# Kernel tuning notes

Hardware: AMD Instinct MI355X
Metric: run time of the kernel (lower is better)

The kernel has to match this reference:

```python
import jax, jax.numpy as jnp
import numpy as np
import math

N_NODES = 25000
N_EDGES = 400000
FEAT = 128
N_RBF = 20
CUTOFF = 5.0
EPS = 1e-15


def setup_inputs() -> dict:
    key = jax.random.key(0)
    ks = jax.random.split(key, 10)
    s_j = jax.random.normal(ks[0], (N_NODES, FEAT), dtype=jnp.float32)
    v_j = jax.random.normal(ks[1], (N_NODES, FEAT, 3), dtype=jnp.float32)
    r_ij = jax.random.normal(ks[2], (N_EDGES, 3), dtype=jnp.float32)
    nbrs = jax.random.randint(ks[3], (N_EDGES, 2), 0, N_NODES, dtype=jnp.int64)
    # InvariantDense: Linear(F,F) -> swish -> Linear(F,3F)
    sc1 = 1.0 / math.sqrt(FEAT)
    W1 = jax.random.uniform(ks[4], (FEAT, FEAT), jnp.float32, -sc1, sc1)
    b1 = jnp.zeros((FEAT,), jnp.float32)
    W2 = jax.random.uniform(ks[5], (FEAT, 3 * FEAT), jnp.float32, -sc1, sc1)
    b2 = jnp.zeros((3 * FEAT,), jnp.float32)
    # DistanceEmbed dense: Linear(n_rbf, 3F)
    scd = 1.0 / math.sqrt(N_RBF)
    Wd = jax.random.uniform(ks[6], (N_RBF, 3 * FEAT), jnp.float32, -scd, scd)
    bd = jnp.zeros((3 * FEAT,), jnp.float32)
    return {"s_j": s_j, "v_j": v_j, "r_ij": r_ij, "nbrs": nbrs,
            "W1": W1, "b1": b1, "W2": W2, "b2": b2, "Wd": Wd, "bd": bd}


def _swish(x):
    return x * jax.nn.sigmoid(x)


def reference(s_j, v_j, r_ij, nbrs, W1, b1, W2, b2, Wd, bd):
    # preprocess_r
    dist = jnp.sqrt(jnp.sum(r_ij * r_ij + EPS, axis=-1))        # [E]
    unit = r_ij / dist[:, None]                                  # [E, 3]

    src = nbrs[:, 1]
    dst = nbrs[:, 0]

    # invariant dense on gathered scalar features
    s_nb = s_j[src]                                              # [E, F]
    phi = _swish(s_nb @ W1 + b1) @ W2 + b2                       # [E, 3F]

    # radial basis: sin(n*pi*d/cutoff)/d, n = 1..n_rbf
    n = jnp.arange(1, N_RBF + 1, dtype=jnp.float32)
    rbf = jnp.sin(n * jnp.pi / CUTOFF * dist[:, None]) / dist[:, None]  # [E, n_rbf]
    w_s = rbf @ Wd + bd                                          # [E, 3F]

    inv = (phi * w_s).reshape(-1, FEAT, 3)                       # [E, F, 3]
    split0 = inv[:, :, 0:1]                                      # [E, F, 1]
    split1 = inv[:, :, 1]                                        # [E, F]
    split2 = inv[:, :, 2:3]                                      # [E, F, 1]

    delta_v_ij = split2 * unit[:, None, :] + split0 * v_j[src]   # [E, F, 3]
    delta_s_ij = split1                                          # [E, F]

    delta_s_i = jax.ops.segment_sum(delta_s_ij, dst, num_segments=s_j.shape[0])
    delta_v_i = jax.ops.segment_sum(delta_v_ij, dst, num_segments=s_j.shape[0])
    return (delta_s_i, delta_v_i)
```

## Files before the change

### kernel.cpp

```cpp
#include <hip/hip_runtime.h>

namespace {

constexpr int FEAT   = 128;
constexpr int NRBF   = 20;
constexpr int EPB    = 32;
constexpr int NNODES = 25000;
constexpr int NEDGES = 400000;
constexpr int NBLK   = NEDGES / EPB;
constexpr int NSCAN  = (NNODES + 255) / 256;
constexpr float PI_F = 3.14159265358979323846f;

using f32x4 = __attribute__((ext_vector_type(4))) float;
using s16x8 = __attribute__((ext_vector_type(8))) short;
using s16x4 = __attribute__((ext_vector_type(4))) short;

constexpr int PW1_ELEMS = 8  * 4 * 64 * 8;
constexpr int PW2_ELEMS = 24 * 4 * 64 * 8;
constexpr int PWD_ELEMS = 24 * 1 * 64 * 8;
constexpr int PW1_OFF = 0;
constexpr int PW2_OFF = PW1_ELEMS;
constexpr int PWD_OFF = PW1_ELEMS + PW2_ELEMS;
constexpr int PT_TOTAL = PW1_ELEMS + PW2_ELEMS + PWD_ELEMS;

__device__ inline unsigned short f2bf(float f) {
    unsigned u = __builtin_bit_cast(unsigned, f);
    u += 0x7fffu + ((u >> 16) & 1u);
    return (unsigned short)(u >> 16);
}
__device__ inline float bf2f(unsigned short h) {
    unsigned u = ((unsigned)h) << 16;
    return __builtin_bit_cast(float, u);
}

__global__ __launch_bounds__(256) void prep_kernel(
    const float* __restrict__ W1, const float* __restrict__ W2,
    const float* __restrict__ Wd, short* __restrict__ pw)
{
    const int idx = blockIdx.x * 256 + threadIdx.x;
    if (idx >= PT_TOTAL) return;
    float val;
    if (idx < PW2_OFF) {
        const int t = idx;
        const int r = t & 7, lane = (t >> 3) & 63, ks = (t >> 9) & 3, nt = t >> 11;
        const int k = ks*32 + (lane>>4)*8 + r, n = nt*16 + (lane & 15);
        val = W1[k*128 + n];
    } else if (idx < PWD_OFF) {
        const int t = idx - PW2_OFF;
        const int r = t & 7, lane = (t >> 3) & 63, ks = (t >> 9) & 3, nt = t >> 11;
        const int k = ks*32 + (lane>>4)*8 + r, n = nt*16 + (lane & 15);
        const int orig = 3*(n & 127) + (n >> 7);
        val = W2[k*384 + orig];
    } else {
        const int t = idx - PWD_OFF;
        const int r = t & 7, lane = (t >> 3) & 63, nt = t >> 9;
        const int k = (lane>>4)*8 + r, n = nt*16 + (lane & 15);
        const int orig = 3*(n & 127) + (n >> 7);
        val = (k < NRBF) ? Wd[k*384 + orig] : 0.f;
    }
    pw[idx] = (short)f2bf(val);
}

__global__ __launch_bounds__(256) void hist_kernel(
    const int* __restrict__ nbrs, int* __restrict__ hist)
{
    const int e = blockIdx.x * 256 + threadIdx.x;
    if (e >= NEDGES) return;
    const int2 nb = reinterpret_cast<const int2*>(nbrs)[e];
    atomicAdd(&hist[nb.x], 1);
}

__global__ __launch_bounds__(256) void scanA_kernel(
    const int* __restrict__ hist, int* __restrict__ cursor, int* __restrict__ bsum)
{
    __shared__ int sh[256];
    const int t = threadIdx.x, idx = blockIdx.x*256 + t;
    const int v = (idx < NNODES) ? hist[idx] : 0;
    sh[t] = v; __syncthreads();
    int acc = v;
    for (int off = 1; off < 256; off <<= 1) {
        const int add = (t >= off) ? sh[t-off] : 0;
        __syncthreads();
        acc += add; sh[t] = acc;
        __syncthreads();
    }
    if (idx < NNODES) cursor[idx] = acc - v;
    if (t == 255) bsum[blockIdx.x] = acc;
}

__global__ __launch_bounds__(128) void scanB_kernel(
    const int* __restrict__ bsum, int* __restrict__ boffs)
{
    __shared__ int sh[128];
    const int t = threadIdx.x;
    const int v = (t < NSCAN) ? bsum[t] : 0;
    sh[t] = v; __syncthreads();
    int acc = v;
    for (int off = 1; off < 128; off <<= 1) {
        const int add = (t >= off) ? sh[t-off] : 0;
        __syncthreads();
        acc += add; sh[t] = acc;
        __syncthreads();
    }
    if (t < NSCAN) boffs[t] = acc - v;
}

__global__ __launch_bounds__(256) void scanC_kernel(
    int* __restrict__ cursor, const int* __restrict__ boffs)
{
    const int idx = blockIdx.x*256 + threadIdx.x;
    if (idx < NNODES) cursor[idx] += boffs[blockIdx.x];
}

__global__ __launch_bounds__(256) void scatter_kernel(
    const int* __restrict__ nbrs, int* __restrict__ cursor,
    int* __restrict__ eids)
{
    const int e = blockIdx.x * 256 + threadIdx.x;
    if (e >= NEDGES) return;
    const int dst = nbrs[2*e];
    const int pos = atomicAdd(&cursor[dst], 1);
    eids[pos] = e;
}

__global__ __launch_bounds__(256) void msg_kernel(
    const float* __restrict__ s_j, const float* __restrict__ v_j,
    const float* __restrict__ r_ij, const int* __restrict__ nbrs,
    const float* __restrict__ b1, const float* __restrict__ b2,
    const float* __restrict__ bd, const short* __restrict__ pw,
    const int* __restrict__ eids,
    float* __restrict__ ds_out, float* __restrict__ dv_out)
{
    __shared__ short sTile[12288];
    __shared__ float sU[EPB][3];
    __shared__ int   sSrc[EPB], sDst[EPB];
    constexpr int OFF_A = 0, OFF_H = 4096, OFF_R = 8192;

    const int tid = threadIdx.x;
    const int w   = tid >> 6;
    const int l   = tid & 63;
    const int mr  = l & 15;
    const int g   = l >> 4;
    const int e0  = blockIdx.x * EPB;

    {
        const int ep  = tid >> 3;
        const int sub = tid & 7;
        const int eid = eids[e0 + ep];
        const int2 nb = reinterpret_cast<const int2*>(nbrs)[eid];
        const float r0 = r_ij[3*eid+0], r1 = r_ij[3*eid+1], r2 = r_ij[3*eid+2];
        const float d     = sqrtf(r0*r0 + r1*r1 + r2*r2 + 3e-15f);
        const float inv_d = 1.0f / d;
        if (sub == 0) {
            sDst[ep] = nb.x; sSrc[ep] = nb.y;
            sU[ep][0] = r0*inv_d; sU[ep][1] = r1*inv_d; sU[ep][2] = r2*inv_d;
        }
        s16x8 rv;
        #pragma unroll
        for (int kk = 0; kk < 8; ++kk) {
            const int k = sub*8 + kk;
            const float v = (k < NRBF) ? __sinf((float)(k+1)*(PI_F/5.0f)*d)*inv_d : 0.f;
            rv[kk] = (short)f2bf(v);
        }
        *reinterpret_cast<s16x8*>(&sTile[OFF_R + ep*64 + ((sub*8) ^ ((ep & 7) << 3))]) = rv;
    }

    #pragma unroll
    for (int p = 0; p < 4; ++p) {
        const int v  = tid + p*256;
        const int e  = v >> 5;
        const int c4 = (v & 31) * 4;
        const int eid = eids[e0 + e];
        const int src = nbrs[2*eid + 1];
        const float4 f = reinterpret_cast<const float4*>(s_j + (size_t)src*FEAT)[v & 31];
        s16x4 h;
        h.x = (short)f2bf(f.x); h.y = (short)f2bf(f.y);
        h.z = (short)f2bf(f.z); h.w = (short)f2bf(f.w);
        *reinterpret_cast<s16x4*>(&sTile[OFF_A + e*128 + (c4 ^ ((e & 7) << 3))]) = h;
    }
    __syncthreads();

    {
        s16x8 aS[2][4];
        #pragma unroll
        for (int mt = 0; mt < 2; ++mt) {
            const int m = mt*16 + mr;
            const int xr = (m & 7) << 3;
            #pragma unroll
            for (int ks = 0; ks < 4; ++ks)
                aS[mt][ks] = *reinterpret_cast<const s16x8*>(&sTile[OFF_A + m*128 + ((ks*32 + g*8) ^ xr)]);
        }
        const s16x8* pW1 = reinterpret_cast<const s16x8*>(pw + PW1_OFF);
        #pragma unroll
        for (int i = 0; i < 2; ++i) {
            const int nt = w*2 + i;
            const int n  = nt*16 + mr;
            const float b1n = b1[n];
            f32x4 acc[2] = {f32x4{0,0,0,0}, f32x4{0,0,0,0}};
            #pragma unroll
            for (int ks = 0; ks < 4; ++ks) {
                const s16x8 b = pW1[(nt*4 + ks)*64 + l];
                acc[0] = __builtin_amdgcn_mfma_f32_16x16x32_bf16(aS[0][ks], b, acc[0], 0, 0, 0);
                acc[1] = __builtin_amdgcn_mfma_f32_16x16x32_bf16(aS[1][ks], b, acc[1], 0, 0, 0);
            }
            #pragma unroll
            for (int mt = 0; mt < 2; ++mt)
                #pragma unroll
                for (int r = 0; r < 4; ++r) {
                    const int m = mt*16 + g*4 + r;
                    const float x = acc[mt][r] + b1n;
                    const float hsw = x / (1.0f + __expf(-x));
                    sTile[OFF_H + m*128 + (n ^ ((m & 7) << 3))] = (short)f2bf(hsw);
                }
        }
    }
    __syncthreads();

    {
        s16x8 aH[2][4], aR[2];
        #pragma unroll
        for (int mt = 0; mt < 2; ++mt) {
            const int m = mt*16 + mr;
            const int xr = (m & 7) << 3;
            #pragma unroll
            for (int ks = 0; ks < 4; ++ks)
                aH[mt][ks] = *reinterpret_cast<const s16x8*>(&sTile[OFF_H + m*128 + ((ks*32 + g*8) ^ xr)]);
            aR[mt] = *reinterpret_cast<const s16x8*>(&sTile[OFF_R + m*64 + ((g*8) ^ xr)]);
        }
        __syncthreads();

        const s16x8* pW2 = reinterpret_cast<const s16x8*>(pw + PW2_OFF);
        const s16x8* pWd = reinterpret_cast<const s16x8*>(pw + PWD_OFF);
        #pragma unroll
        for (int i = 0; i < 6; ++i) {
            const int nt = w*6 + i;
            const int n  = nt*16 + mr;
            const int c  = n >> 7;
            const int f2 = n & 127;
            const int orig = 3*f2 + c;
            const float b2n = b2[orig], bdn = bd[orig];
            f32x4 acc[2]  = {f32x4{0,0,0,0}, f32x4{0,0,0,0}};
            f32x4 accw[2] = {f32x4{0,0,0,0}, f32x4{0,0,0,0}};
            #pragma unroll
            for (int ks = 0; ks < 4; ++ks) {
                const s16x8 b = pW2[(nt*4 + ks)*64 + l];
                acc[0] = __builtin_amdgcn_mfma_f32_16x16x32_bf16(aH[0][ks], b, acc[0], 0, 0, 0);
                acc[1] = __builtin_amdgcn_mfma_f32_16x16x32_bf16(aH[1][ks], b, acc[1], 0, 0, 0);
            }
            const s16x8 bw = pWd[nt*64 + l];
            accw[0] = __builtin_amdgcn_mfma_f32_16x16x32_bf16(aR[0], bw, accw[0], 0, 0, 0);
            accw[1] = __builtin_amdgcn_mfma_f32_16x16x32_bf16(aR[1], bw, accw[1], 0, 0, 0);
            #pragma unroll
            for (int mt = 0; mt < 2; ++mt)
                #pragma unroll
                for (int r = 0; r < 4; ++r) {
                    const int m = mt*16 + g*4 + r;
                    const float inv = (acc[mt][r] + b2n) * (accw[mt][r] + bdn);
                    sTile[c*4096 + m*128 + (f2 ^ ((m & 7) << 3))] = (short)f2bf(inv);
                }
        }
    }
    __syncthreads();

    {
        const int half = tid >> 7;
        const int f    = tid & 127;
        const int eb   = half * 16;
        float accS = 0.f, a0 = 0.f, a1 = 0.f, a2 = 0.f;
        int cur = sDst[eb];
        #pragma unroll 4
        for (int e = eb; e < eb + 16; ++e) {
            const int d = sDst[e];
            if (d != cur) {
                atomicAdd(ds_out + (size_t)cur*FEAT + f, accS);
                float* dvp = dv_out + (size_t)cur*(3*FEAT) + 3*f;
                atomicAdd(dvp + 0, a0);
                atomicAdd(dvp + 1, a1);
                atomicAdd(dvp + 2, a2);
                accS = a0 = a1 = a2 = 0.f;
                cur = d;
            }
            const int fx = f ^ ((e & 7) << 3);
            const float i0 = bf2f((unsigned short)sTile[        e*128 + fx]);
            const float i1 = bf2f((unsigned short)sTile[4096 + e*128 + fx]);
            const float i2 = bf2f((unsigned short)sTile[8192 + e*128 + fx]);
            const int src = sSrc[e];
            const float* vj = v_j + (size_t)src*(3*FEAT) + 3*f;
            const float u0 = sU[e][0], u1 = sU[e][1], u2 = sU[e][2];
            accS += i1;
            a0 += i2*u0 + i0*vj[0];
            a1 += i2*u1 + i0*vj[1];
            a2 += i2*u2 + i0*vj[2];
        }
        atomicAdd(ds_out + (size_t)cur*FEAT + f, accS);
        float* dvp = dv_out + (size_t)cur*(3*FEAT) + 3*f;
        atomicAdd(dvp + 0, a0);
        atomicAdd(dvp + 1, a1);
        atomicAdd(dvp + 2, a2);
    }
}

}

extern "C" void kernel_launch(void* const* d_in, const int* in_sizes, int n_in,
                              void* d_out, int out_size, void* d_ws, size_t ws_size,
                              hipStream_t stream)
{
    const float* s_j  = (const float*)d_in[0];
    const float* v_j  = (const float*)d_in[1];
    const float* r_ij = (const float*)d_in[2];
    const int*   nbrs = (const int*)d_in[3];
    const float* W1   = (const float*)d_in[4];
    const float* b1   = (const float*)d_in[5];
    const float* W2   = (const float*)d_in[6];
    const float* b2   = (const float*)d_in[7];
    const float* Wd   = (const float*)d_in[8];
    const float* bd   = (const float*)d_in[9];

    float* ds_out = (float*)d_out;
    float* dv_out = ds_out + (size_t)NNODES * FEAT;

    char* base   = (char*)d_ws;
    short* pw    = (short*)base;
    int*  hist   = (int*)(base + 160*1024);
    int*  cursor = (int*)(base + 272*1024);
    int*  bsum   = (int*)(base + 376*1024);
    int*  boffs  = (int*)(base + 380*1024);
    int*  eids   = (int*)(base + 384*1024);

    hipMemsetAsync(d_out, 0, (size_t)out_size * sizeof(float), stream);
    hipMemsetAsync(hist, 0, NNODES * sizeof(int), stream);

    prep_kernel<<<(PT_TOTAL + 255)/256, 256, 0, stream>>>(W1, W2, Wd, pw);
    hist_kernel<<<(NEDGES + 255)/256, 256, 0, stream>>>(nbrs, hist);
    scanA_kernel<<<NSCAN, 256, 0, stream>>>(hist, cursor, bsum);
    scanB_kernel<<<1, 128, 0, stream>>>(bsum, boffs);
    scanC_kernel<<<NSCAN, 256, 0, stream>>>(cursor, boffs);
    scatter_kernel<<<(NEDGES + 255)/256, 256, 0, stream>>>(nbrs, cursor, eids);

    msg_kernel<<<NBLK, 256, 0, stream>>>(
        s_j, v_j, r_ij, nbrs, b1, b2, bd, pw, eids, ds_out, dv_out);
}
```

Baseline: 438.2 us.

## Compute phi per node instead of per edge and pre-sort edge records

```diff
diff --git a/kernel.cpp b/kernel.cpp
--- a/kernel.cpp
+++ b/kernel.cpp
@@ -8,6 +8,7 @@
 constexpr int NNODES = 25000;
 constexpr int NEDGES = 400000;
 constexpr int NBLK   = NEDGES / EPB;
+constexpr int NPBLK  = (NNODES + 31) / 32;
 constexpr int NSCAN  = (NNODES + 255) / 256;
 constexpr float PI_F = 3.14159265358979323846f;
 
@@ -61,6 +62,111 @@
     pw[idx] = (short)f2bf(val);
 }
 
+__global__ __launch_bounds__(256) void nodephi_kernel(
+    const float* __restrict__ s_j, const float* __restrict__ b1,
+    const float* __restrict__ b2, const short* __restrict__ pw,
+    unsigned short* __restrict__ phiT)
+{
+    __shared__ short sT[8192];
+    constexpr int OFF_H = 4096;
+    const int tid = threadIdx.x;
+    const int w   = tid >> 6;
+    const int l   = tid & 63;
+    const int mr  = l & 15;
+    const int g   = l >> 4;
+    const int n0  = blockIdx.x * 32;
+
+    #pragma unroll
+    for (int p = 0; p < 4; ++p) {
+        const int v  = tid + p*256;
+        const int e  = v >> 5;
+        const int c4 = (v & 31) * 4;
+        const int node = n0 + e;
+        float4 f = {0.f, 0.f, 0.f, 0.f};
+        if (node < NNODES)
+            f = reinterpret_cast<const float4*>(s_j + (size_t)node*FEAT)[v & 31];
+        s16x4 h;
+        h.x = (short)f2bf(f.x); h.y = (short)f2bf(f.y);
+        h.z = (short)f2bf(f.z); h.w = (short)f2bf(f.w);
+        *reinterpret_cast<s16x4*>(&sT[e*128 + (c4 ^ ((e & 7) << 3))]) = h;
+    }
+    __syncthreads();
+
+    {
+        s16x8 aS[2][4];
+        #pragma unroll
+        for (int mt = 0; mt < 2; ++mt) {
+            const int m = mt*16 + mr;
+            const int xr = (m & 7) << 3;
+            #pragma unroll
+            for (int ks = 0; ks < 4; ++ks)
+                aS[mt][ks] = *reinterpret_cast<const s16x8*>(&sT[m*128 + ((ks*32 + g*8) ^ xr)]);
+        }
+        const s16x8* pW1 = reinterpret_cast<const s16x8*>(pw + PW1_OFF);
+        #pragma unroll
+        for (int i = 0; i < 2; ++i) {
+            const int nt = w*2 + i;
+            const int n  = nt*16 + mr;
+            const float b1n = b1[n];
+            f32x4 acc[2] = {f32x4{0,0,0,0}, f32x4{0,0,0,0}};
+            #pragma unroll
+            for (int ks = 0; ks < 4; ++ks) {
+                const s16x8 b = pW1[(nt*4 + ks)*64 + l];
+                acc[0] = __builtin_amdgcn_mfma_f32_16x16x32_bf16(aS[0][ks], b, acc[0], 0, 0, 0);
+                acc[1] = __builtin_amdgcn_mfma_f32_16x16x32_bf16(aS[1][ks], b, acc[1], 0, 0, 0);
+            }
+            #pragma unroll
+            for (int mt = 0; mt < 2; ++mt)
+                #pragma unroll
+                for (int r = 0; r < 4; ++r) {
+                    const int m = mt*16 + g*4 + r;
+                    const float x = acc[mt][r] + b1n;
+                    const float hsw = x / (1.0f + __expf(-x));
+                    sT[OFF_H + m*128 + (n ^ ((m & 7) << 3))] = (short)f2bf(hsw);
+                }
+        }
+    }
+    __syncthreads();
+
+    {
+        s16x8 aH[2][4];
+        #pragma unroll
+        for (int mt = 0; mt < 2; ++mt) {
+            const int m = mt*16 + mr;
+            const int xr = (m & 7) << 3;
+            #pragma unroll
+            for (int ks = 0; ks < 4; ++ks)
+                aH[mt][ks] = *reinterpret_cast<const s16x8*>(&sT[OFF_H + m*128 + ((ks*32 + g*8) ^ xr)]);
+        }
+        const s16x8* pW2 = reinterpret_cast<const s16x8*>(pw + PW2_OFF);
+        #pragma unroll
+        for (int i = 0; i < 6; ++i) {
+            const int nt = w*6 + i;
+            const int n  = nt*16 + mr;
+            const int c  = n >> 7;
+            const int f2 = n & 127;
+            const float b2n = b2[3*f2 + c];
+            f32x4 acc[2] = {f32x4{0,0,0,0}, f32x4{0,0,0,0}};
+            #pragma unroll
+            for (int ks = 0; ks < 4; ++ks) {
+                const s16x8 b = pW2[(nt*4 + ks)*64 + l];
+                acc[0] = __builtin_amdgcn_mfma_f32_16x16x32_bf16(aH[0][ks], b, acc[0], 0, 0, 0);
+                acc[1] = __builtin_amdgcn_mfma_f32_16x16x32_bf16(aH[1][ks], b, acc[1], 0, 0, 0);
+            }
+            #pragma unroll
+            for (int mt = 0; mt < 2; ++mt)
+                #pragma unroll
+                for (int r = 0; r < 4; ++r) {
+                    const int m = mt*16 + g*4 + r;
+                    const int node = n0 + m;
+                    if (node < NNODES)
+                        phiT[(size_t)c*NNODES*FEAT + (size_t)node*FEAT + f2] =
+                            f2bf(acc[mt][r] + b2n);
+                }
+        }
+    }
+}
+
 __global__ __launch_bounds__(256) void hist_kernel(
     const int* __restrict__ nbrs, int* __restrict__ hist)
 {
@@ -113,28 +219,27 @@
 }
 
 __global__ __launch_bounds__(256) void scatter_kernel(
-    const int* __restrict__ nbrs, int* __restrict__ cursor,
-    int* __restrict__ eids)
+    const int* __restrict__ nbrs, const float* __restrict__ r_ij,
+    int* __restrict__ cursor, int2* __restrict__ recDS, float4* __restrict__ recR)
 {
     const int e = blockIdx.x * 256 + threadIdx.x;
     if (e >= NEDGES) return;
-    const int dst = nbrs[2*e];
-    const int pos = atomicAdd(&cursor[dst], 1);
-    eids[pos] = e;
+    const int2 nb = reinterpret_cast<const int2*>(nbrs)[e];
+    const int pos = atomicAdd(&cursor[nb.x], 1);
+    recDS[pos] = nb;
+    recR[pos] = make_float4(r_ij[3*e+0], r_ij[3*e+1], r_ij[3*e+2], 0.f);
 }
 
 __global__ __launch_bounds__(256) void msg_kernel(
-    const float* __restrict__ s_j, const float* __restrict__ v_j,
-    const float* __restrict__ r_ij, const int* __restrict__ nbrs,
-    const float* __restrict__ b1, const float* __restrict__ b2,
-    const float* __restrict__ bd, const short* __restrict__ pw,
-    const int* __restrict__ eids,
+    const float* __restrict__ v_j, const int2* __restrict__ recDS,
+    const float4* __restrict__ recR, const float* __restrict__ bd,
+    const short* __restrict__ pw, const unsigned short* __restrict__ phiT,
     float* __restrict__ ds_out, float* __restrict__ dv_out)
 {
-    __shared__ short sTile[12288];
+    __shared__ short sP[14336];
     __shared__ float sU[EPB][3];
     __shared__ int   sSrc[EPB], sDst[EPB];
-    constexpr int OFF_A = 0, OFF_H = 4096, OFF_R = 8192;
+    constexpr int OFF_R = 12288;
 
     const int tid = threadIdx.x;
     const int w   = tid >> 6;
@@ -146,14 +251,13 @@
     {
         const int ep  = tid >> 3;
         const int sub = tid & 7;
-        const int eid = eids[e0 + ep];
-        const int2 nb = reinterpret_cast<const int2*>(nbrs)[eid];
-        const float r0 = r_ij[3*eid+0], r1 = r_ij[3*eid+1], r2 = r_ij[3*eid+2];
-        const float d     = sqrtf(r0*r0 + r1*r1 + r2*r2 + 3e-15f);
+        const int2  nb = recDS[e0 + ep];
+        const float4 r = recR[e0 + ep];
+        const float d     = sqrtf(r.x*r.x + r.y*r.y + r.z*r.z + 3e-15f);
         const float inv_d = 1.0f / d;
         if (sub == 0) {
             sDst[ep] = nb.x; sSrc[ep] = nb.y;
-            sU[ep][0] = r0*inv_d; sU[ep][1] = r1*inv_d; sU[ep][2] = r2*inv_d;
+            sU[ep][0] = r.x*inv_d; sU[ep][1] = r.y*inv_d; sU[ep][2] = r.z*inv_d;
         }
         s16x8 rv;
         #pragma unroll
@@ -162,74 +266,31 @@
             const float v = (k < NRBF) ? __sinf((float)(k+1)*(PI_F/5.0f)*d)*inv_d : 0.f;
             rv[kk] = (short)f2bf(v);
         }
-        *reinterpret_cast<s16x8*>(&sTile[OFF_R + ep*64 + ((sub*8) ^ ((ep & 7) << 3))]) = rv;
+        *reinterpret_cast<s16x8*>(&sP[OFF_R + ep*64 + ((sub*8) ^ ((ep & 7) << 3))]) = rv;
     }
 
     #pragma unroll
-    for (int p = 0; p < 4; ++p) {
-        const int v  = tid + p*256;
-        const int e  = v >> 5;
-        const int c4 = (v & 31) * 4;
-        const int eid = eids[e0 + e];
-        const int src = nbrs[2*eid + 1];
-        const float4 f = reinterpret_cast<const float4*>(s_j + (size_t)src*FEAT)[v & 31];
-        s16x4 h;
-        h.x = (short)f2bf(f.x); h.y = (short)f2bf(f.y);
-        h.z = (short)f2bf(f.z); h.w = (short)f2bf(f.w);
-        *reinterpret_cast<s16x4*>(&sTile[OFF_A + e*128 + (c4 ^ ((e & 7) << 3))]) = h;
+    for (int pl = 0; pl < 3; ++pl) {
+        #pragma unroll
+        for (int p = 0; p < 2; ++p) {
+            const int v  = tid + p*256;
+            const int e  = v >> 4;
+            const int ch = (v & 15) * 8;
+            const int src = recDS[e0 + e].y;
+            const s16x8 val = *reinterpret_cast<const s16x8*>(
+                phiT + (size_t)pl*NNODES*FEAT + (size_t)src*FEAT + ch);
+            *reinterpret_cast<s16x8*>(&sP[pl*4096 + e*128 + (ch ^ ((e & 7) << 3))]) = val;
+        }
     }
     __syncthreads();
 
     {
-        s16x8 aS[2][4];
+        s16x8 aR[2];
         #pragma unroll
         for (int mt = 0; mt < 2; ++mt) {
             const int m = mt*16 + mr;
-            const int xr = (m & 7) << 3;
-            #pragma unroll
-            for (int ks = 0; ks < 4; ++ks)
-                aS[mt][ks] = *reinterpret_cast<const s16x8*>(&sTile[OFF_A + m*128 + ((ks*32 + g*8) ^ xr)]);
-        }
-        const s16x8* pW1 = reinterpret_cast<const s16x8*>(pw + PW1_OFF);
-        #pragma unroll
-        for (int i = 0; i < 2; ++i) {
-            const int nt = w*2 + i;
-            const int n  = nt*16 + mr;
-            const float b1n = b1[n];
-            f32x4 acc[2] = {f32x4{0,0,0,0}, f32x4{0,0,0,0}};
-            #pragma unroll
-            for (int ks = 0; ks < 4; ++ks) {
-                const s16x8 b = pW1[(nt*4 + ks)*64 + l];
-                acc[0] = __builtin_amdgcn_mfma_f32_16x16x32_bf16(aS[0][ks], b, acc[0], 0, 0, 0);
-                acc[1] = __builtin_amdgcn_mfma_f32_16x16x32_bf16(aS[1][ks], b, acc[1], 0, 0, 0);
-            }
-            #pragma unroll
-            for (int mt = 0; mt < 2; ++mt)
-                #pragma unroll
-                for (int r = 0; r < 4; ++r) {
-                    const int m = mt*16 + g*4 + r;
-                    const float x = acc[mt][r] + b1n;
-                    const float hsw = x / (1.0f + __expf(-x));
-                    sTile[OFF_H + m*128 + (n ^ ((m & 7) << 3))] = (short)f2bf(hsw);
-                }
-        }
-    }
-    __syncthreads();
-
-    {
-        s16x8 aH[2][4], aR[2];
-        #pragma unroll
-        for (int mt = 0; mt < 2; ++mt) {
-            const int m = mt*16 + mr;
-            const int xr = (m & 7) << 3;
-            #pragma unroll
-            for (int ks = 0; ks < 4; ++ks)
-                aH[mt][ks] = *reinterpret_cast<const s16x8*>(&sTile[OFF_H + m*128 + ((ks*32 + g*8) ^ xr)]);
-            aR[mt] = *reinterpret_cast<const s16x8*>(&sTile[OFF_R + m*64 + ((g*8) ^ xr)]);
-        }
-        __syncthreads();
-
-        const s16x8* pW2 = reinterpret_cast<const s16x8*>(pw + PW2_OFF);
+            aR[mt] = *reinterpret_cast<const s16x8*>(&sP[OFF_R + m*64 + ((g*8) ^ ((m & 7) << 3))]);
+        }
         const s16x8* pWd = reinterpret_cast<const s16x8*>(pw + PWD_OFF);
         #pragma unroll
         for (int i = 0; i < 6; ++i) {
@@ -237,17 +298,9 @@
             const int n  = nt*16 + mr;
             const int c  = n >> 7;
             const int f2 = n & 127;
-            const int orig = 3*f2 + c;
-            const float b2n = b2[orig], bdn = bd[orig];
-            f32x4 acc[2]  = {f32x4{0,0,0,0}, f32x4{0,0,0,0}};
+            const float bdn = bd[3*f2 + c];
+            const s16x8 bw = pWd[nt*64 + l];
             f32x4 accw[2] = {f32x4{0,0,0,0}, f32x4{0,0,0,0}};
-            #pragma unroll
-            for (int ks = 0; ks < 4; ++ks) {
-                const s16x8 b = pW2[(nt*4 + ks)*64 + l];
-                acc[0] = __builtin_amdgcn_mfma_f32_16x16x32_bf16(aH[0][ks], b, acc[0], 0, 0, 0);
-                acc[1] = __builtin_amdgcn_mfma_f32_16x16x32_bf16(aH[1][ks], b, acc[1], 0, 0, 0);
-            }
-            const s16x8 bw = pWd[nt*64 + l];
             accw[0] = __builtin_amdgcn_mfma_f32_16x16x32_bf16(aR[0], bw, accw[0], 0, 0, 0);
             accw[1] = __builtin_amdgcn_mfma_f32_16x16x32_bf16(aR[1], bw, accw[1], 0, 0, 0);
             #pragma unroll
@@ -255,8 +308,9 @@
                 #pragma unroll
                 for (int r = 0; r < 4; ++r) {
                     const int m = mt*16 + g*4 + r;
-                    const float inv = (acc[mt][r] + b2n) * (accw[mt][r] + bdn);
-                    sTile[c*4096 + m*128 + (f2 ^ ((m & 7) << 3))] = (short)f2bf(inv);
+                    const int addr = c*4096 + m*128 + (f2 ^ ((m & 7) << 3));
+                    const float phi = bf2f((unsigned short)sP[addr]);
+                    sP[addr] = (short)f2bf(phi * (accw[mt][r] + bdn));
                 }
         }
     }
@@ -281,9 +335,9 @@
                 cur = d;
             }
             const int fx = f ^ ((e & 7) << 3);
-            const float i0 = bf2f((unsigned short)sTile[        e*128 + fx]);
-            const float i1 = bf2f((unsigned short)sTile[4096 + e*128 + fx]);
-            const float i2 = bf2f((unsigned short)sTile[8192 + e*128 + fx]);
+            const float i0 = bf2f((unsigned short)sP[        e*128 + fx]);
+            const float i1 = bf2f((unsigned short)sP[4096 + e*128 + fx]);
+            const float i2 = bf2f((unsigned short)sP[8192 + e*128 + fx]);
             const int src = sSrc[e];
             const float* vj = v_j + (size_t)src*(3*FEAT) + 3*f;
             const float u0 = sU[e][0], u1 = sU[e][1], u2 = sU[e][2];
@@ -320,24 +374,27 @@
     float* ds_out = (float*)d_out;
     float* dv_out = ds_out + (size_t)NNODES * FEAT;
 
-    char* base   = (char*)d_ws;
-    short* pw    = (short*)base;
-    int*  hist   = (int*)(base + 160*1024);
-    int*  cursor = (int*)(base + 272*1024);
-    int*  bsum   = (int*)(base + 376*1024);
-    int*  boffs  = (int*)(base + 380*1024);
-    int*  eids   = (int*)(base + 384*1024);
+    char* base = (char*)d_ws;
+    short* pw            = (short*)base;
+    int*   hist          = (int*)(base + 160*1024);
+    int*   cursor        = (int*)(base + 272*1024);
+    int*   bsum          = (int*)(base + 376*1024);
+    int*   boffs         = (int*)(base + 380*1024);
+    int2*  recDS         = (int2*)(base + 512*1024);
+    float4* recR         = (float4*)(base + 4ull*1024*1024);
+    unsigned short* phiT = (unsigned short*)(base + 16ull*1024*1024);
 
     hipMemsetAsync(d_out, 0, (size_t)out_size * sizeof(float), stream);
     hipMemsetAsync(hist, 0, NNODES * sizeof(int), stream);
 
     prep_kernel<<<(PT_TOTAL + 255)/256, 256, 0, stream>>>(W1, W2, Wd, pw);
+    nodephi_kernel<<<NPBLK, 256, 0, stream>>>(s_j, b1, b2, pw, phiT);
     hist_kernel<<<(NEDGES + 255)/256, 256, 0, stream>>>(nbrs, hist);
     scanA_kernel<<<NSCAN, 256, 0, stream>>>(hist, cursor, bsum);
     scanB_kernel<<<1, 128, 0, stream>>>(bsum, boffs);
     scanC_kernel<<<NSCAN, 256, 0, stream>>>(cursor, boffs);
-    scatter_kernel<<<(NEDGES + 255)/256, 256, 0, stream>>>(nbrs, cursor, eids);
+    scatter_kernel<<<(NEDGES + 255)/256, 256, 0, stream>>>(nbrs, r_ij, cursor, recDS, recR);
 
     msg_kernel<<<NBLK, 256, 0, stream>>>(
-        s_j, v_j, r_ij, nbrs, b1, b2, bd, pw, eids, ds_out, dv_out);
-}
+        v_j, recDS, recR, bd, pw, phiT, ds_out, dv_out);
+}
```

Result: faster. 408.6 us (-6.7%).
